# Kernel optimization log

Hardware: AMD Instinct MI355X
Metric: run time of the kernel (lower is better)

The kernel has to match this reference:

```python
import jax, jax.numpy as jnp
import numpy as np

N = 8192      # num nodes
D = 128       # feature dim (input_dim)
E = 262144    # num edges (avg degree 32)
P = 4         # num perspectives (num_pers)
EPSILON = 0.3 # similarity threshold (args.epsilon)


def setup_inputs() -> dict:
    key = jax.random.key(0)
    k1, k2, k3, k4 = jax.random.split(key, 4)
    x = jax.random.normal(k1, (N, D), dtype=jnp.float32)
    ori_index = jax.random.randint(k2, (2, E), 0, N, dtype=jnp.int32)
    ori_weight = jax.random.uniform(k3, (E,), dtype=jnp.float32)
    w_pers = jax.random.normal(k4, (P, D), dtype=jnp.float32)  # weighted-cosine perspective weights
    return {"x": x, "ori_index": ori_index, "ori_weight": ori_weight, "w_pers": w_pers}


def reference(x, ori_index, ori_weight, w_pers):
    n = x.shape[0]
    # to_dense_adj: scatter edge weights into dense [N, N] adjacency (duplicate edges add)
    ori_g = jnp.zeros((n, n), dtype=x.dtype).at[ori_index[0], ori_index[1]].add(ori_weight)

    # GraphLearner (weighted multi-perspective cosine):
    # reweight features per perspective, L2-normalize, cosine sim, mean over perspectives
    xw = x[None, :, :] * w_pers[:, None, :]                              # [P, N, D]
    xn = xw / jnp.maximum(jnp.linalg.norm(xw, axis=-1, keepdims=True), 1e-12)
    sim = jnp.mean(jnp.einsum('pnd,pmd->pnm', xn, xn), axis=0)           # [N, N]
    # epsilon-thresholded learned graph
    sim_g = jnp.where(sim > EPSILON, sim, jnp.zeros_like(sim))

    # purified(sim, ori_g, epsilon): keep original edges where sim*ori_g > epsilon
    pur_g = jnp.where(sim * ori_g > EPSILON, ori_g, jnp.zeros_like(sim))
    new_g = pur_g + sim_g
    # dense_to_sparse has data-dependent output size; return the dense refined
    # adjacency (same information: edges = nonzero(new_g), weights = values).
    return new_g
```

## Files before the change

kernel.cpp:

```cpp
#include <hip/hip_runtime.h>
#include <hip/hip_bf16.h>
#include <stdint.h>

#define N_NODES 8192
#define DIM     128
#define KTOT    512
#define NEDGE   262144
#define EPS     0.3f
#define FIX_DELTA 0.008f
#define FIX_CAP (1u << 19)
#define XCAP    (1u << 18)
#define LCAP    512
#define HASH_BITS 19
#define HASH_SLOTS (1u << HASH_BITS)

typedef unsigned int u32;
typedef unsigned short u16;
typedef __attribute__((ext_vector_type(8))) short short8;
typedef __attribute__((ext_vector_type(4))) float float4v;

#define OFF_YF  0u
#define OFF_YB  16777216u
#define OFF_CTR 25165824u
#define OFF_HK  25166080u
#define OFF_HV  27263232u
#define OFF_FL  29360384u
#define OFF_UL  31457536u
#define OFF_XL  32506112u
#define MEMSET_OFF OFF_CTR
#define MEMSET_BYTES (OFF_FL - OFF_CTR)

__device__ __forceinline__ u16 f2bf(float f) {
    u32 b = __builtin_bit_cast(u32, f);
    b += 0x7fffu + ((b >> 16) & 1u);
    return (u16)(b >> 16);
}

__global__ void prep_y(const float* __restrict__ x, const float* __restrict__ wp,
                       float* __restrict__ yf, u16* __restrict__ yb) {
    int node = blockIdx.x * 4 + (threadIdx.x >> 6);
    int lane = threadIdx.x & 63;
    float x0 = x[node * DIM + lane];
    float x1 = x[node * DIM + lane + 64];
    for (int p = 0; p < 4; ++p) {
        float v0 = x0 * wp[p * DIM + lane];
        float v1 = x1 * wp[p * DIM + lane + 64];
        float ss = v0 * v0 + v1 * v1;
        #pragma unroll
        for (int o = 1; o < 64; o <<= 1) ss += __shfl_xor(ss, o, 64);
        float scale = 0.5f / fmaxf(sqrtf(ss), 1e-12f);
        float y0 = v0 * scale, y1 = v1 * scale;
        int base = node * KTOT + p * DIM;
        yf[base + lane] = y0;       yf[base + lane + 64] = y1;
        yb[base + lane] = f2bf(y0); yb[base + lane + 64] = f2bf(y1);
    }
}

__global__ void edge_insert(const int* __restrict__ idx, const float* __restrict__ w,
                            u32* __restrict__ hkey, float* __restrict__ hval,
                            u32* __restrict__ ucnt, u32* __restrict__ ulist) {
    int e = blockIdx.x * 256 + threadIdx.x;
    u32 cell = (u32)(idx[e] * N_NODES + idx[NEDGE + e]);
    float wv = w[e];
    u32 key = cell + 1u;
    u32 h = (cell * 2654435761u) >> (32 - HASH_BITS);
    while (true) {
        u32 old = atomicCAS(&hkey[h], 0u, key);
        if (old == 0u) { ulist[atomicAdd(ucnt, 1u)] = h; atomicAdd(&hval[h], wv); break; }
        if (old == key) { atomicAdd(&hval[h], wv); break; }
        h = (h + 1u) & (HASH_SLOTS - 1u);
    }
}

#define TM  128
#define BK  64

__global__ __launch_bounds__(256)
void gemm_sim(const u16* __restrict__ yb, float* __restrict__ out,
              u32* __restrict__ fcnt, u32* __restrict__ flst) {
    __shared__ __align__(16) u16 As[TM * BK];
    __shared__ __align__(16) u16 Bs[TM * BK];
    __shared__ u32 s_cnt, s_base;
    __shared__ u32 s_list[LCAP];
    int bm = blockIdx.y, bn = blockIdx.x;
    int tid = threadIdx.x;
    int lane = tid & 63, wid = tid >> 6;
    int wm = wid >> 1, wn = wid & 1;
    if (tid == 0) s_cnt = 0;

    float4v acc[4][4] = {};
    const u16* arow = yb + (size_t)(bm * TM) * KTOT;
    const u16* brow = yb + (size_t)(bn * TM) * KTOT;

    for (int kt = 0; kt < KTOT / BK; ++kt) {
        __syncthreads();
        #pragma unroll
        for (int q = 0; q < 4; ++q) {
            int c = q * 256 + wid * 64 + lane;
            int row = c >> 3;
            int kg = (c & 7) ^ (row & 7);
            __builtin_amdgcn_global_load_lds(
                (const __attribute__((address_space(1))) void*)(const void*)(arow + (size_t)row * KTOT + kt * BK + kg * 8),
                (__attribute__((address_space(3))) void*)(void*)(As + (q * 256 + wid * 64) * 8),
                16, 0, 0);
            __builtin_amdgcn_global_load_lds(
                (const __attribute__((address_space(1))) void*)(const void*)(brow + (size_t)row * KTOT + kt * BK + kg * 8),
                (__attribute__((address_space(3))) void*)(void*)(Bs + (q * 256 + wid * 64) * 8),
                16, 0, 0);
        }
        __syncthreads();
        #pragma unroll
        for (int kk = 0; kk < 2; ++kk) {
            short8 af[4], bfr[4];
            int kg2 = kk * 4 + (lane >> 4);
            int mrow = wm * 64 + (lane & 15);
            int ncol = wn * 64 + (lane & 15);
            #pragma unroll
            for (int i = 0; i < 4; ++i) {
                int ra = mrow + i * 16, rb = ncol + i * 16;
                af[i]  = *(const short8*)&As[ra * BK + ((kg2 ^ (ra & 7)) * 8)];
                bfr[i] = *(const short8*)&Bs[rb * BK + ((kg2 ^ (rb & 7)) * 8)];
            }
            #pragma unroll
            for (int i = 0; i < 4; ++i)
                #pragma unroll
                for (int j = 0; j < 4; ++j)
                    acc[i][j] = __builtin_amdgcn_mfma_f32_16x16x32_bf16(
                        af[i], bfr[j], acc[i][j], 0, 0, 0);
        }
    }

    int quad = lane >> 4, lcol = lane & 15;
    #pragma unroll
    for (int i = 0; i < 4; ++i)
        #pragma unroll
        for (int j = 0; j < 4; ++j) {
            int gr0 = bm * TM + wm * 64 + i * 16 + quad * 4;
            int gc  = bn * TM + wn * 64 + j * 16 + lcol;
            #pragma unroll
            for (int r = 0; r < 4; ++r) {
                float s = acc[i][j][r];
                out[(size_t)(gr0 + r) * N_NODES + gc] = s > EPS ? s : 0.f;
                if (fabsf(s - EPS) < FIX_DELTA) {
                    u32 li = atomicAdd(&s_cnt, 1u);
                    u32 cell = (u32)((gr0 + r) * N_NODES + gc);
                    if (li < LCAP) s_list[li] = cell;
                    else { u32 g = atomicAdd(fcnt, 1u); if (g < FIX_CAP) flst[g] = cell; }
                }
            }
        }
    __syncthreads();
    u32 cnt = s_cnt < LCAP ? s_cnt : LCAP;
    if (tid == 0) s_base = atomicAdd(fcnt, cnt);
    __syncthreads();
    for (u32 t = tid; t < cnt; t += 256) {
        u32 g = s_base + t;
        if (g < FIX_CAP) flst[g] = s_list[t];
    }
}

__device__ __forceinline__ float dot_exact(const float* __restrict__ yf,
                                           u32 i, u32 j, int tl) {
    const float4v* ri = (const float4v*)(yf + (size_t)i * KTOT);
    const float4v* rj = (const float4v*)(yf + (size_t)j * KTOT);
    float4v p = {};
    #pragma unroll
    for (int q = 0; q < 8; ++q) p += ri[q * 16 + tl] * rj[q * 16 + tl];
    float s = p.x + p.y + p.z + p.w;
    #pragma unroll
    for (int o = 8; o >= 1; o >>= 1) s += __shfl_xor(s, o, 16);
    return s;
}

__global__ void fixup(const float* __restrict__ yf, const u32* __restrict__ fcnt,
                      const u32* __restrict__ flst, float* __restrict__ out) {
    u32 count = *fcnt; if (count > FIX_CAP) count = FIX_CAP;
    int team = (blockIdx.x * 256 + threadIdx.x) >> 4;
    int tl = threadIdx.x & 15;
    int nteams = gridDim.x * 16;
    for (u32 t = team; t < count; t += nteams) {
        u32 cell = flst[t];
        u32 i = cell >> 13, j = cell & 8191u;
        float s = dot_exact(yf, i, j, tl);
        if (tl == 0) out[cell] = s > EPS ? s : 0.f;
    }
}

__global__ void edge_fast(const u32* __restrict__ hkey, const float* __restrict__ hval,
                          const u32* __restrict__ ucnt, const u32* __restrict__ ulist,
                          float* __restrict__ out,
                          u32* __restrict__ xcnt, u32* __restrict__ xlist) {
    u32 count = *ucnt;
    for (u32 t = blockIdx.x * 256 + threadIdx.x; t < count; t += gridDim.x * 256) {
        u32 h = ulist[t];
        u32 cell = hkey[h] - 1u;
        float a = hval[h];
        float sg = out[cell];
        bool hard = (a > 1.0f) ||
                    (sg > 0.f && fabsf(sg * a - EPS) < FIX_DELTA * a + 1e-6f) ||
                    (sg == 0.f && a > 0.97f);
        if (hard) {
            u32 g = atomicAdd(xcnt, 1u);
            if (g < XCAP) xlist[g] = h;
        } else if (sg > 0.f) {
            out[cell] = sg + ((sg * a > EPS) ? a : 0.f);
        }
    }
}

__global__ void edge_exact(const float* __restrict__ yf, const u32* __restrict__ hkey,
                           const float* __restrict__ hval, const u32* __restrict__ xcnt,
                           const u32* __restrict__ xlist, float* __restrict__ out) {
    u32 count = *xcnt; if (count > XCAP) count = XCAP;
    int team = (blockIdx.x * 256 + threadIdx.x) >> 4;
    int tl = threadIdx.x & 15;
    int nteams = gridDim.x * 16;
    for (u32 t = team; t < count; t += nteams) {
        u32 h = xlist[t];
        u32 cell = hkey[h] - 1u;
        float a = hval[h];
        u32 i = cell >> 13, j = cell & 8191u;
        float s = dot_exact(yf, i, j, tl);
        if (tl == 0) {
            float v = s > EPS ? s : 0.f;
            if (s * a > EPS) v += a;
            out[cell] = v;
        }
    }
}

extern "C" void kernel_launch(void* const* d_in, const int* in_sizes, int n_in,
                              void* d_out, int out_size, void* d_ws, size_t ws_size,
                              hipStream_t stream) {
    const float* x  = (const float*)d_in[0];
    const int*   oi = (const int*)d_in[1];
    const float* ow = (const float*)d_in[2];
    const float* wp = (const float*)d_in[3];
    float* out = (float*)d_out;
    char* ws = (char*)d_ws;
    float* yf = (float*)(ws + OFF_YF);
    u16*   yb = (u16*)(ws + OFF_YB);
    u32*   fc = (u32*)(ws + OFF_CTR);
    u32*   uc = (u32*)(ws + OFF_CTR + 4);
    u32*   xc = (u32*)(ws + OFF_CTR + 8);
    u32*   hk = (u32*)(ws + OFF_HK);
    float* hv = (float*)(ws + OFF_HV);
    u32*   fl = (u32*)(ws + OFF_FL);
    u32*   ul = (u32*)(ws + OFF_UL);
    u32*   xl = (u32*)(ws + OFF_XL);

    prep_y<<<N_NODES / 4, 256, 0, stream>>>(x, wp, yf, yb);
    hipMemsetAsync(ws + MEMSET_OFF, 0, MEMSET_BYTES, stream);
    edge_insert<<<NEDGE / 256, 256, 0, stream>>>(oi, ow, hk, hv, uc, ul);
    gemm_sim<<<dim3(N_NODES / TM, N_NODES / TM), 256, 0, stream>>>(yb, out, fc, fl);
    fixup<<<2048, 256, 0, stream>>>(yf, fc, fl, out);
    edge_fast<<<1024, 256, 0, stream>>>(hk, hv, uc, ul, out, xc, xl);
    edge_exact<<<256, 256, 0, stream>>>(yf, hk, hv, xc, xl, out);
}
```

Measured before the change: 526.2 us.

## Exploit similarity symmetry: compute upper-triangle tiles and mirror via LDS transpose

```diff
diff --git a/kernel.cpp b/kernel.cpp
--- a/kernel.cpp
+++ b/kernel.cpp
@@ -74,15 +74,19 @@
 
 #define TM  128
 #define BK  64
+#define TLD 132
 
 __global__ __launch_bounds__(256)
 void gemm_sim(const u16* __restrict__ yb, float* __restrict__ out,
               u32* __restrict__ fcnt, u32* __restrict__ flst) {
-    __shared__ __align__(16) u16 As[TM * BK];
-    __shared__ __align__(16) u16 Bs[TM * BK];
+    int bm = blockIdx.y, bn = blockIdx.x;
+    if (bm > bn) return;
+    __shared__ __align__(16) char smem[64 * TLD * 4];
+    u16* As = (u16*)smem;
+    u16* Bs = As + TM * BK;
+    float* tbuf = (float*)smem;
     __shared__ u32 s_cnt, s_base;
     __shared__ u32 s_list[LCAP];
-    int bm = blockIdx.y, bn = blockIdx.x;
     int tid = threadIdx.x;
     int lane = tid & 63, wid = tid >> 6;
     int wm = wid >> 1, wn = wid & 1;
@@ -142,13 +146,46 @@
                 float s = acc[i][j][r];
                 out[(size_t)(gr0 + r) * N_NODES + gc] = s > EPS ? s : 0.f;
                 if (fabsf(s - EPS) < FIX_DELTA) {
-                    u32 li = atomicAdd(&s_cnt, 1u);
-                    u32 cell = (u32)((gr0 + r) * N_NODES + gc);
-                    if (li < LCAP) s_list[li] = cell;
-                    else { u32 g = atomicAdd(fcnt, 1u); if (g < FIX_CAP) flst[g] = cell; }
+                    u32 cellA = (u32)((gr0 + r) * N_NODES + gc);
+                    u32 cellB = (u32)(gc * N_NODES + (gr0 + r));
+                    u32 li = atomicAdd(&s_cnt, 2u);
+                    if (li + 1 < LCAP) { s_list[li] = cellA; s_list[li + 1] = cellB; }
+                    else {
+                        u32 g = atomicAdd(fcnt, 2u);
+                        if (g < FIX_CAP) flst[g] = cellA;
+                        if (g + 1 < FIX_CAP) flst[g + 1] = cellB;
+                    }
                 }
             }
         }
+
+    #pragma unroll
+    for (int h = 0; h < 2; ++h) {
+        __syncthreads();
+        if (wn == h) {
+            #pragma unroll
+            for (int i = 0; i < 4; ++i) {
+                int Lr = wm * 64 + i * 16 + quad * 4;
+                #pragma unroll
+                for (int j = 0; j < 4; ++j) {
+                    int Lc = j * 16 + lcol;
+                    *(float4v*)&tbuf[Lc * TLD + Lr] = acc[i][j];
+                }
+            }
+        }
+        __syncthreads();
+        #pragma unroll
+        for (int v = 0; v < 8; ++v) {
+            int chunk = v * 256 + tid;
+            int row = chunk >> 5, c4 = chunk & 31;
+            float4v t = *(const float4v*)&tbuf[row * TLD + c4 * 4];
+            float4v o;
+            #pragma unroll
+            for (int r = 0; r < 4; ++r) o[r] = t[r] > EPS ? t[r] : 0.f;
+            *(float4v*)&out[(size_t)(bn * TM + h * 64 + row) * N_NODES + bm * TM + c4 * 4] = o;
+        }
+    }
+
     __syncthreads();
     u32 cnt = s_cnt < LCAP ? s_cnt : LCAP;
     if (tid == 0) s_base = atomicAdd(fcnt, cnt);
```

Measured after the change: 495.8 us. 5.8% less time.
